# Performance work log

Hardware: AMD Instinct MI355X
Metric: run time of the kernel (lower is better)

## Reference

```python
import jax, jax.numpy as jnp
import numpy as np

N = 20000; E = 160000; C = 64; SH = 9; NB = 8
S_DIM = 16; MS_HID = 64; FC_HID = 64
RATE = 0.1; LAMBDA = 0.5; R_MAX = 5.0; EV_PER = 16
K = int(RATE * N)          # static master-node count (top-k selection)
E_V = EV_PER * K           # static virtual-edge budget


def _safe_len(vec):
    # smooth norm, safe under autodiff at zero-length edges (self loops)
    return jnp.sqrt(jnp.sum(vec * vec, axis=-1, keepdims=True) + 1e-12)


def _sh(vec):
    # real spherical harmonics lmax=2, 'component' normalization, on unit vectors
    n = vec / _safe_len(vec)
    x, y, z = n[:, 0], n[:, 1], n[:, 2]
    s3 = jnp.sqrt(3.0); s15 = jnp.sqrt(15.0); s5 = jnp.sqrt(5.0)
    return jnp.stack([
        jnp.ones_like(x),
        s3 * x, s3 * y, s3 * z,
        s15 * x * y, s15 * y * z, 0.5 * s5 * (3 * z * z - 1.0),
        s15 * x * z, 0.5 * s15 * (x * x - y * y),
    ], axis=-1)  # [E, 9]


def _bessel(r):
    # Bessel radial basis with p=6 polynomial cutoff envelope; r: [E,1]
    n = jnp.arange(1, NB + 1, dtype=r.dtype)
    b = jnp.sqrt(2.0 / R_MAX) * jnp.sin(n * jnp.pi * r / R_MAX) / jnp.clip(r, 1e-9)
    u = jnp.clip(r / R_MAX, 0.0, 1.0); p = 6.0
    env = 1.0 - (p + 1) * (p + 2) / 2 * u ** p + p * (p + 2) * u ** (p + 1) - p * (p + 1) / 2 * u ** (p + 2)
    return b * env  # [E, NB]


def _conv(h, src, dst, sh, ef, emask, n_nodes, fc_w1, fc_b1, fc_w2, fc_b2, lin_w):
    # TFN-style tensor-product conv: per-edge weights from radial MLP,
    # message = flatten(h[dst] outer sh) * w -> linear -> scatter-mean to src
    w = jax.nn.relu(ef @ fc_w1 + fc_b1) @ fc_w2 + fc_b2            # [E, C*SH]
    tp = (h[dst][:, :, None] * sh[:, None, :]).reshape(sh.shape[0], -1) * w
    msg = (tp @ lin_w) * emask[:, None]                            # [E, C]
    agg = jax.ops.segment_sum(msg, src, num_segments=n_nodes)
    deg = jax.ops.segment_sum(emask, src, num_segments=n_nodes)
    return agg / jnp.clip(deg, 1.0)[:, None]


def setup_inputs() -> dict:
    key = jax.random.key(0)
    ks = jax.random.split(key, 12)
    def lin(k, i, o):
        return (jax.random.normal(k, (i, o), jnp.float32) / np.sqrt(i)).astype(jnp.float32)
    return {
        "h": jax.random.normal(ks[0], (N, C), jnp.float32),
        "pos": jax.random.uniform(ks[1], (N, 3), jnp.float32) * 10.0,
        "edge_index": jax.random.randint(ks[2], (2, E), 0, N, dtype=jnp.int32),
        "fc_w1": lin(ks[3], NB, FC_HID), "fc_b1": jnp.zeros((FC_HID,), jnp.float32),
        "fc_w2": lin(ks[4], FC_HID, C * SH), "fc_b2": jnp.zeros((C * SH,), jnp.float32),
        "lin_w": lin(ks[5], C * SH, C),
        "ms_w1": lin(ks[6], S_DIM, MS_HID), "ms_b1": jnp.zeros((MS_HID,), jnp.float32),
        "ms_w2": lin(ks[7], MS_HID, 1), "ms_b2": jnp.zeros((1,), jnp.float32),
        "vg_wq": lin(ks[8], S_DIM, S_DIM), "vg_wk": lin(ks[9], S_DIM, S_DIM),
    }


def reference(h, pos, fc_w1, fc_b1, fc_w2, fc_b2, lin_w,
              ms_w1, ms_b1, ms_w2, ms_b2, vg_wq, vg_wk, edge_index):
    src, dst = edge_index[0], edge_index[1]
    vec = pos[src] - pos[dst]
    sh = _sh(vec)
    ef = _bessel(_safe_len(vec))
    ones_e = jnp.ones((E,), h.dtype)
    h_update = _conv(h, src, dst, sh, ef, ones_e, N, fc_w1, fc_b1, fc_w2, fc_b2, lin_w)
    h_local = h_update + h  # in_dim == out_dim -> pad is a no-op

    # --- master selection (top-k by learned score; static K) ---
    h_sc = h_local[:, :S_DIM]
    score = jax.nn.sigmoid(
        (jax.nn.relu(h_sc @ ms_w1 + ms_b1) @ ms_w2 + ms_b2).squeeze(-1))  # [N]
    _, top_idx = jax.lax.top_k(score, K)
    node_mask = jnp.zeros((N,), h.dtype).at[top_idx].set(1.0)
    m = score * node_mask
    master_idx = jnp.sort(top_idx)

    # relabel full-graph ids -> master-subgraph ids (masked subgraph extraction)
    node2m = jnp.full((N,), -1, jnp.int32).at[master_idx].set(jnp.arange(K, dtype=jnp.int32))
    src_m, dst_m = node2m[src], node2m[dst]
    e_mask = ((src_m >= 0) & (dst_m >= 0)).astype(h.dtype)
    src_mc = jnp.where(src_m >= 0, src_m, 0)
    dst_mc = jnp.where(dst_m >= 0, dst_m, 0)
    adj = jnp.zeros((K, K), h.dtype).at[src_mc, dst_mc].add(e_mask)

    h_master = h_local[master_idx]
    pos_master = pos[master_idx]
    h_ms = h_master[:, :S_DIM]

    # --- virtual edge generation (attention, thresholded by lambda) ---
    q = h_ms @ vg_wq; kk = h_ms @ vg_wk
    attn = jax.nn.sigmoid(q @ kk.T / np.sqrt(S_DIM))  # [K, K]
    exist = (adj > 0) | jnp.eye(K, dtype=bool)
    A_virtual = jnp.where((~exist) & (attn > LAMBDA), 1.0, 0.0).astype(h.dtype)
    vvals, vidx = jax.lax.top_k((attn * A_virtual).reshape(-1), E_V)
    v_src = (vidx // K).astype(jnp.int32); v_dst = (vidx % K).astype(jnp.int32)
    v_mask = (vvals > 0).astype(h.dtype)

    src_all = jnp.concatenate([src_mc, v_src])
    dst_all = jnp.concatenate([dst_mc, v_dst])
    mask_all = jnp.concatenate([e_mask, v_mask])
    vec_m = pos_master[src_all] - pos_master[dst_all]
    sh_m = _sh(vec_m)
    ef_m = _bessel(_safe_len(vec_m))
    h_m_update = _conv(h_master, src_all, dst_all, sh_m, ef_m, mask_all, K,
                       fc_w1, fc_b1, fc_w2, fc_b2, lin_w)
    h_hier = h_m_update + h_master

    h_hier_exp = jnp.zeros_like(h_local).at[master_idx].set(h_hier)
    m_e = m[:, None]
    h_final = (1.0 - m_e) * h_local + m_e * h_hier_exp
    return (h_final, pos, A_virtual, m)
```

## Files before the change

kernel.cpp:

```cpp
#include <hip/hip_runtime.h>
#include <stdint.h>

constexpr int N_   = 20000;
constexpr int E_   = 160000;
constexpr int C_   = 64;
constexpr int K_   = 2000;
constexpr int EV_  = 32000;
constexpr int EALL_ = E_ + EV_;
constexpr int CSH_ = 576;
constexpr int TB_  = 64;
constexpr int NFLAT_ = K_ * K_;

constexpr size_t OFF_AGG    = 0;
constexpr size_t OFF_DEG    = 5120000;
constexpr size_t OFF_AGGM   = 5200000;
constexpr size_t OFF_DEGM   = 5712000;
constexpr size_t OFF_RANK   = 5720000;
constexpr size_t OFF_MASKA  = 5800000;
constexpr size_t OFF_EXIST  = 6568000;
constexpr size_t OFF_HIST   = 10568000;
constexpr size_t OFF_STATE  = 10572096;
constexpr size_t OFF_HLOCAL = 10572352;
constexpr size_t OFF_KEY    = 15692352;
constexpr size_t OFF_SCORE  = 15852352;
constexpr size_t OFF_N2M    = 15932352;
constexpr size_t OFF_MIDX   = 16012352;
constexpr size_t OFF_HM     = 16020352;
constexpr size_t OFF_POSM   = 16532352;
constexpr size_t OFF_Q      = 16556352;
constexpr size_t OFF_KBUF   = 16684352;
constexpr size_t OFF_SRCA   = 16812352;
constexpr size_t OFF_DSTA   = 17580352;
constexpr size_t OFF_WMAX   = 18348352;
constexpr size_t OFF_CAND   = 18598400;

struct RState {
    unsigned long long prefix;
    int R;
    unsigned int cand_count;
    unsigned int sel_count;
    int bin_thresh;
    unsigned int total;
    unsigned int pad;
};

__global__ __launch_bounds__(256) void k_init(const float* __restrict__ fc_b1,
    const float* __restrict__ fc_w2, const float* __restrict__ fc_b2, char* __restrict__ ws)
{
    float4 zero4 = make_float4(0.f, 0.f, 0.f, 0.f);
    float4* z = (float4*)ws;
    int nz4 = (int)(OFF_STATE / 16);
    for (int i = blockIdx.x * 256 + threadIdx.x; i < nz4; i += gridDim.x * 256) z[i] = zero4;
    if (blockIdx.x == gridDim.x - 1) {
        __shared__ float hid0[64];
        __shared__ int nz;
        int t = threadIdx.x;
        float4* zs = (float4*)(ws + OFF_STATE);
        if (t < 16) zs[t] = zero4;
        if (t == 0) nz = 0;
        if (t < 64) hid0[t] = fmaxf(fc_b1[t], 0.0f);
        __syncthreads();
        for (int j = t; j < CSH_; j += 256) {
            float acc = fc_b2[j];
            for (int k = 0; k < 64; k++) acc += hid0[k] * fc_w2[k * CSH_ + j];
            if (acc != 0.0f) atomicOr(&nz, 1);
        }
        __syncthreads();
        if (t == 0) *(int*)(ws + OFF_STATE + 72) = nz;
    }
}

__global__ __launch_bounds__(256) void k_prep(
    int n_edges, const int* __restrict__ src, const int* __restrict__ dst,
    const float* __restrict__ mask, const float* __restrict__ posn,
    const int* __restrict__ w0nz, float* __restrict__ deg,
    float* __restrict__ edata, unsigned int* __restrict__ cnt)
{
    int e = blockIdx.x * 256 + threadIdx.x;
    bool valid = e < n_edges;
    int s_i = 0, d_i = 0; float msk = 0.0f;
    if (valid) {
        msk = mask ? mask[e] : 1.0f;
        if (msk != 0.0f) { s_i = src[e]; d_i = dst[e]; }
    }
    bool active = valid && (msk != 0.0f);

    float vx = 0.f, vy = 0.f, vz = 0.f;
    if (active) {
        vx = posn[s_i*3+0] - posn[d_i*3+0];
        vy = posn[s_i*3+1] - posn[d_i*3+1];
        vz = posn[s_i*3+2] - posn[d_i*3+2];
    }
    float r = sqrtf(vx*vx + vy*vy + vz*vz + 1e-12f);
    float invr = 1.0f / r;
    float x = vx*invr, y = vy*invr, z = vz*invr;
    const float s3 = 1.7320508075688772f, s15 = 3.872983346207417f, s5 = 2.23606797749979f;
    float sh[9];
    sh[0] = 1.0f; sh[1] = s3*x; sh[2] = s3*y; sh[3] = s3*z;
    sh[4] = s15*x*y; sh[5] = s15*y*z; sh[6] = 0.5f*s5*(3.0f*z*z - 1.0f);
    sh[7] = s15*x*z; sh[8] = 0.5f*s15*(x*x - y*y);

    float u = r * 0.2f; u = u > 1.0f ? 1.0f : u;
    float u2 = u*u, u6 = u2*u2*u2, u7 = u6*u, u8 = u7*u;
    float env = 1.0f - 28.0f*u6 + 48.0f*u7 - 21.0f*u8;
    float rc = r > 1e-9f ? r : 1e-9f;
    const float bpref = 0.6324555320336759f;
    const float PIov5 = 0.6283185307179586f;
    float ef[8];
    #pragma unroll
    for (int n = 0; n < 8; n++)
        ef[n] = bpref * sinf(PIov5 * r * (float)(n + 1)) / rc * env;

    if (active) atomicAdd(&deg[s_i], msk);

    bool contrib = active && !((env == 0.0f) && (*w0nz == 0));
    int lane = threadIdx.x & 63;
    unsigned long long b = __ballot(contrib);
    int wc = __popcll(b);
    int base = 0;
    if (lane == 0 && wc) base = (int)atomicAdd(cnt, (unsigned)wc);
    base = __shfl(base, 0);
    if (contrib) {
        int slot = base + __popcll(b & ((1ull << lane) - 1ull));
        float* p = edata + (size_t)slot * 20;
        #pragma unroll
        for (int n = 0; n < 8; n++) p[n] = ef[n];
        #pragma unroll
        for (int t = 0; t < 9; t++) p[8+t] = sh[t];
        p[17] = __int_as_float(s_i);
        p[18] = __int_as_float(d_i);
        p[19] = msk;
    }
}

__global__ __launch_bounds__(256, 3) void k_convg(
    const unsigned int* __restrict__ cnt, const float* __restrict__ edata,
    const float* __restrict__ hn,
    const float* __restrict__ fc_w1, const float* __restrict__ fc_b1,
    const float* __restrict__ fc_w2, const float* __restrict__ fc_b2,
    const float* __restrict__ lin_w, float* __restrict__ agg)
{
    __shared__ float s_misc[TB_ * 12];
    __shared__ __align__(16) float s_hid[64 * 64];
    __shared__ __align__(16) float s_tp[64 * 68];
    __shared__ __align__(16) float s_w[4096];

    const int tid = threadIdx.x;
    const int oq = (tid & 15) * 4;
    const int e0 = (tid >> 4) * 4;

    const int nheavy = (int)*cnt;
    const int nblk = (nheavy + TB_ - 1) / TB_;

    for (int blk = blockIdx.x; blk < nblk; blk += gridDim.x) {
        const int ebase = blk * TB_;
        int nE = nheavy - ebase; if (nE > TB_) nE = TB_;

        __syncthreads();
        for (int idx = tid; idx < TB_ * 12; idx += 256) {
            int e = idx / 12, f = idx - 12 * e;
            float v = 0.0f;
            if (e < nE) {
                const float* p = edata + (size_t)(ebase + e) * 20;
                v = (f < 9) ? p[8 + f] : (f == 9) ? p[17] : (f == 10) ? p[19] : p[18];
            }
            s_misc[idx] = v;
        }
        for (int idx = tid; idx < TB_ * 64; idx += 256) {
            int k = idx >> 6, e = idx & 63;
            float hv = 0.0f;
            if (e < nE) {
                const float* p = edata + (size_t)(ebase + e) * 20;
                float acc = fc_b1[k];
                #pragma unroll
                for (int n = 0; n < 8; n++) acc += p[n] * fc_w1[n * 64 + k];
                hv = fmaxf(acc, 0.0f);
            }
            s_hid[k * 64 + e] = hv;
        }
        float acc[4][4] = {{0,0,0,0},{0,0,0,0},{0,0,0,0},{0,0,0,0}};
        __syncthreads();

        const int d0 = __float_as_int(s_misc[(e0+0) * 12 + 11]);
        const int d1 = __float_as_int(s_misc[(e0+1) * 12 + 11]);
        const int d2 = __float_as_int(s_misc[(e0+2) * 12 + 11]);
        const int d3 = __float_as_int(s_misc[(e0+3) * 12 + 11]);

        for (int cj = 0; cj < 9; cj++) {
            const int j0 = cj * 64;
            if (cj) __syncthreads();
            for (int i4 = tid; i4 < 1024; i4 += 256) {
                int k = i4 >> 4, q4 = (i4 & 15) * 4;
                *reinterpret_cast<float4*>(&s_w[k * 64 + q4]) =
                    *reinterpret_cast<const float4*>(&fc_w2[k * CSH_ + j0 + q4]);
            }
            __syncthreads();

            const int jb = j0 + oq;
            const int c0 = jb / 9, c1 = (jb + 3) / 9;
            float hA0 = hn[d0 * 64 + c0], hB0 = hn[d0 * 64 + c1];
            float hA1 = hn[d1 * 64 + c0], hB1 = hn[d1 * 64 + c1];
            float hA2 = hn[d2 * 64 + c0], hB2 = hn[d2 * 64 + c1];
            float hA3 = hn[d3 * 64 + c0], hB3 = hn[d3 * 64 + c1];

            float a[4][4];
            #pragma unroll
            for (int q = 0; q < 4; q++) {
                float b = fc_b2[jb + q];
                a[0][q]=b; a[1][q]=b; a[2][q]=b; a[3][q]=b;
            }
            #pragma unroll 4
            for (int k = 0; k < 64; k++) {
                float4 w4 = *reinterpret_cast<const float4*>(&s_w[k * 64 + oq]);
                float4 h4 = *reinterpret_cast<const float4*>(&s_hid[k * 64 + e0]);
                a[0][0]+=h4.x*w4.x; a[0][1]+=h4.x*w4.y; a[0][2]+=h4.x*w4.z; a[0][3]+=h4.x*w4.w;
                a[1][0]+=h4.y*w4.x; a[1][1]+=h4.y*w4.y; a[1][2]+=h4.y*w4.z; a[1][3]+=h4.y*w4.w;
                a[2][0]+=h4.z*w4.x; a[2][1]+=h4.z*w4.y; a[2][2]+=h4.z*w4.z; a[2][3]+=h4.z*w4.w;
                a[3][0]+=h4.w*w4.x; a[3][1]+=h4.w*w4.y; a[3][2]+=h4.w*w4.z; a[3][3]+=h4.w*w4.w;
            }
            #pragma unroll
            for (int q = 0; q < 4; q++) {
                int j = jb + q; int cc = j / 9; int si = j - 9 * cc;
                float4 tpv;
                tpv.x = (cc == c0 ? hA0 : hB0) * s_misc[(e0+0) * 12 + si] * a[0][q];
                tpv.y = (cc == c0 ? hA1 : hB1) * s_misc[(e0+1) * 12 + si] * a[1][q];
                tpv.z = (cc == c0 ? hA2 : hB2) * s_misc[(e0+2) * 12 + si] * a[2][q];
                tpv.w = (cc == c0 ? hA3 : hB3) * s_misc[(e0+3) * 12 + si] * a[3][q];
                *reinterpret_cast<float4*>(&s_tp[(oq + q) * 68 + e0]) = tpv;
            }
            __syncthreads();

            for (int i4 = tid; i4 < 1024; i4 += 256) {
                *reinterpret_cast<float4*>(&s_w[i4 * 4]) =
                    *reinterpret_cast<const float4*>(&lin_w[j0 * 64 + i4 * 4]);
            }
            __syncthreads();

            #pragma unroll 4
            for (int jj = 0; jj < 64; jj++) {
                float4 l4 = *reinterpret_cast<const float4*>(&s_w[jj * 64 + oq]);
                float4 t4 = *reinterpret_cast<const float4*>(&s_tp[jj * 68 + e0]);
                acc[0][0]+=t4.x*l4.x; acc[0][1]+=t4.x*l4.y; acc[0][2]+=t4.x*l4.z; acc[0][3]+=t4.x*l4.w;
                acc[1][0]+=t4.y*l4.x; acc[1][1]+=t4.y*l4.y; acc[1][2]+=t4.y*l4.z; acc[1][3]+=t4.y*l4.w;
                acc[2][0]+=t4.z*l4.x; acc[2][1]+=t4.z*l4.y; acc[2][2]+=t4.z*l4.z; acc[2][3]+=t4.z*l4.w;
                acc[3][0]+=t4.w*l4.x; acc[3][1]+=t4.w*l4.y; acc[3][2]+=t4.w*l4.z; acc[3][3]+=t4.w*l4.w;
            }
        }

        #pragma unroll
        for (int t = 0; t < 4; t++) {
            float mk = s_misc[(e0+t) * 12 + 10];
            if (mk != 0.0f) {
                int s = __float_as_int(s_misc[(e0+t) * 12 + 9]);
                #pragma unroll
                for (int q = 0; q < 4; q++) atomicAdd(&agg[s * 64 + oq + q], acc[t][q] * mk);
            }
        }
    }
}

__global__ __launch_bounds__(256) void k_hlscore(const float* __restrict__ h,
    const float* __restrict__ agg, const float* __restrict__ deg,
    const float* __restrict__ ms_w1, const float* __restrict__ ms_b1,
    const float* __restrict__ ms_w2, const float* __restrict__ ms_b2,
    float* __restrict__ h_local, float* __restrict__ score, unsigned long long* __restrict__ key)
{
    int wid = threadIdx.x >> 6, lane = threadIdx.x & 63;
    int n = blockIdx.x * 4 + wid;
    if (n >= N_) return;
    float d = fmaxf(deg[n], 1.0f);
    float hl = h[n*64 + lane] + agg[n*64 + lane] / d;
    h_local[n*64 + lane] = hl;
    float acc = ms_b1[lane];
    #pragma unroll
    for (int i = 0; i < 16; i++) acc += __shfl(hl, i) * ms_w1[i*64 + lane];
    acc = fmaxf(acc, 0.0f);
    float part = acc * ms_w2[lane];
    #pragma unroll
    for (int off = 32; off > 0; off >>= 1) part += __shfl_xor(part, off);
    if (lane == 0) {
        float s = part + ms_b2[0];
        float sc = 1.0f / (1.0f + expf(-s));
        score[n] = sc;
        key[n] = ((unsigned long long)__float_as_uint(sc) << 32)
               | (unsigned long long)(0xFFFFFFFFu - (unsigned)n);
    }
}

__global__ __launch_bounds__(256) void k_rank(const unsigned long long* __restrict__ key,
                                              int* __restrict__ rankcnt)
{
    int i = blockIdx.x * 256 + threadIdx.x;
    int seg = blockIdx.y;
    int lo = seg * 1250, hi = lo + 1250;
    unsigned long long my = (i < N_) ? key[i] : ~0ull;
    int cnt = 0;
    #pragma unroll 8
    for (int j = lo; j < hi; j++) cnt += (key[j] > my) ? 1 : 0;
    if (i < N_ && cnt) atomicAdd(&rankcnt[i], cnt);
}

__global__ __launch_bounds__(1024) void k_scanfin(const int* __restrict__ rankcnt,
    const float* __restrict__ score, int* __restrict__ node2m, int* __restrict__ midx,
    float* __restrict__ m_out)
{
    __shared__ int wsum[16];
    __shared__ int wbase[16];
    __shared__ int s_base;
    int tid = threadIdx.x, lane = tid & 63, wv = tid >> 6;
    if (tid == 0) s_base = 0;
    __syncthreads();
    for (int c = 0; c < 20; c++) {
        int idx = c * 1024 + tid;
        int sel = 0;
        if (idx < N_) {
            sel = (rankcnt[idx] < K_) ? 1 : 0;
            m_out[idx] = sel ? score[idx] : 0.0f;
        }
        int v = sel;
        #pragma unroll
        for (int off = 1; off < 64; off <<= 1) {
            int u = __shfl_up(v, off);
            if (lane >= off) v += u;
        }
        if (lane == 63) wsum[wv] = v;
        __syncthreads();
        if (tid == 0) {
            int runb = s_base;
            for (int w = 0; w < 16; w++) { wbase[w] = runb; runb += wsum[w]; }
            s_base = runb;
        }
        __syncthreads();
        if (idx < N_) {
            if (sel) { int rk = wbase[wv] + v - 1; node2m[idx] = rk; midx[rk] = idx; }
            else node2m[idx] = -1;
        }
    }
}

__global__ __launch_bounds__(256) void k_mastex(const int* __restrict__ midx,
    const float* __restrict__ h_local, const float* __restrict__ pos,
    const float* __restrict__ vg_wq, const float* __restrict__ vg_wk,
    const int* __restrict__ src, const int* __restrict__ dst, const int* __restrict__ node2m,
    float* __restrict__ h_m, float* __restrict__ pos_m,
    float* __restrict__ qbuf, float* __restrict__ kbuf,
    int* __restrict__ src_all, int* __restrict__ dst_all,
    float* __restrict__ mask_all, unsigned char* __restrict__ exist)
{
    int b = blockIdx.x;
    if (b < 500) {
        int mi = b * 4 + (threadIdx.x >> 6);
        int lane = threadIdx.x & 63;
        int node = midx[mi];
        h_m[mi*64 + lane] = h_local[node*64 + lane];
        if (lane < 3) pos_m[mi*3 + lane] = pos[node*3 + lane];
        if (lane < 32) {
            int j = lane & 15;
            const float* wm = (lane < 16) ? vg_wq : vg_wk;
            float acc = 0.0f;
            #pragma unroll
            for (int i = 0; i < 16; i++) acc += h_local[node*64 + i] * wm[i*16 + j];
            if (lane < 16) qbuf[mi*16 + j] = acc; else kbuf[mi*16 + j] = acc;
        }
    } else {
        int e = (b - 500) * 256 + threadIdx.x;
        int sm = node2m[src[e]], dm = node2m[dst[e]];
        bool em = (sm >= 0) && (dm >= 0);
        int smc = sm >= 0 ? sm : 0;
        int dmc = dm >= 0 ? dm : 0;
        src_all[e] = smc; dst_all[e] = dmc; mask_all[e] = em ? 1.0f : 0.0f;
        if (em) exist[smc * K_ + dmc] = 1;
    }
}

__global__ __launch_bounds__(256) void k_attn1(const float* __restrict__ qbuf,
    const float* __restrict__ kbuf, const unsigned char* __restrict__ exist,
    float* __restrict__ Av, float* __restrict__ wmax, unsigned int* __restrict__ hist,
    RState* st, unsigned int* __restrict__ done_ctr)
{
    __shared__ unsigned int lh[1024];
    __shared__ unsigned int ha[1024], hb[1024];
    __shared__ unsigned int s_last;
    int tid = threadIdx.x, lane = tid & 63;
    for (int b = tid; b < 1024; b += 256) lh[b] = 0;
    __syncthreads();

    const int stride = gridDim.x * 256;
    for (int flat = blockIdx.x * 256 + tid; flat < NFLAT_; flat += stride) {
        int gi = flat / K_;
        int gj = flat - gi * K_;
        const float4* qp = reinterpret_cast<const float4*>(qbuf + gi * 16);
        const float4* kp = reinterpret_cast<const float4*>(kbuf + gj * 16);
        float dot = 0.0f;
        #pragma unroll
        for (int c4 = 0; c4 < 4; c4++) {
            float4 q4 = qp[c4], k4 = kp[c4];
            dot += q4.x*k4.x + q4.y*k4.y + q4.z*k4.z + q4.w*k4.w;
        }
        float attn = 1.0f / (1.0f + expf(-dot * 0.25f));
        bool ex = (exist[flat] != 0) || (gi == gj);
        bool av = (!ex) && (attn > 0.5f);
        Av[flat] = av ? 1.0f : 0.0f;
        float cv = av ? attn : 0.0f;
        if (av) {
            unsigned bin = (__float_as_uint(attn) - 0x3F000000u) >> 13;
            if (bin > 1023u) bin = 1023u;
            atomicAdd(&lh[bin], 1u);
        }
        float wm = cv;
        #pragma unroll
        for (int off = 32; off > 0; off >>= 1) wm = fmaxf(wm, __shfl_xor(wm, off));
        if (lane == 0) wmax[flat >> 6] = wm;
    }
    __syncthreads();
    for (int b = tid; b < 1024; b += 256) {
        unsigned v = lh[b];
        if (v) atomicAdd(&hist[b], v);
    }
    __syncthreads();
    __threadfence();
    if (tid == 0) s_last = (atomicAdd(done_ctr, 1u) == (unsigned)gridDim.x - 1u) ? 1u : 0u;
    __syncthreads();
    if (!s_last) return;
    __threadfence();
    for (int b = tid; b < 1024; b += 256) ha[b] = atomicAdd(&hist[b], 0u);
    __syncthreads();
    unsigned* srcp = ha; unsigned* dstp = hb;
    for (int off = 1; off < 1024; off <<= 1) {
        for (int b = tid; b < 1024; b += 256)
            dstp[b] = srcp[b] + ((b + off < 1024) ? srcp[b + off] : 0u);
        __syncthreads();
        unsigned* tmp = srcp; srcp = dstp; dstp = tmp;
    }
    unsigned total = srcp[0];
    int R = (total < (unsigned)EV_) ? (int)total : EV_;
    if (tid == 0) {
        st->R = R; st->total = total; st->cand_count = 0; st->sel_count = 0;
        if (R == 0) st->bin_thresh = 1024;
    }
    __syncthreads();
    if (R > 0) {
        for (int b = tid; b < 1024; b += 256) {
            unsigned hi2 = (b == 1023) ? 0u : srcp[b + 1];
            if ((int)srcp[b] >= R && (int)hi2 < R) st->bin_thresh = b;
        }
    }
}

__global__ __launch_bounds__(256) void k_attn2(const float* __restrict__ qbuf,
    const float* __restrict__ kbuf, const unsigned char* __restrict__ exist,
    const float* __restrict__ wmax, RState* st, unsigned long long* __restrict__ cand)
{
    __shared__ int wb[4];
    __shared__ int bb;
    int tid = threadIdx.x, lane = tid & 63, wv = tid >> 6;
    unsigned tbits = 0x3F000000u + ((unsigned)st->bin_thresh << 13);
    const int stride = gridDim.x * 256;

    for (int base = blockIdx.x * 256; base < NFLAT_; base += stride) {
        int flat = base + tid;
        bool wactive = __float_as_uint(wmax[(base + wv * 64) >> 6]) >= tbits;
        bool store = false;
        unsigned long long keyv = 0ull;
        if (wactive) {
            int gi = flat / K_;
            int gj = flat - gi * K_;
            const float4* qp = reinterpret_cast<const float4*>(qbuf + gi * 16);
            const float4* kp = reinterpret_cast<const float4*>(kbuf + gj * 16);
            float dot = 0.0f;
            #pragma unroll
            for (int c4 = 0; c4 < 4; c4++) {
                float4 q4 = qp[c4], k4 = kp[c4];
                dot += q4.x*k4.x + q4.y*k4.y + q4.z*k4.z + q4.w*k4.w;
            }
            float attn = 1.0f / (1.0f + expf(-dot * 0.25f));
            bool ex = (exist[flat] != 0) || (gi == gj);
            store = (!ex) && (attn > 0.5f) && (__float_as_uint(attn) >= tbits);
            keyv = ((unsigned long long)__float_as_uint(attn) << 32)
                 | (unsigned long long)(0xFFFFFFFFu - (unsigned)flat);
        }
        unsigned long long b = __ballot(store);
        int wc = __popcll(b);
        if (lane == 0) wb[wv] = wc;
        __syncthreads();
        if (tid == 0) {
            int s = 0;
            for (int w = 0; w < 4; w++) { int cc2 = wb[w]; wb[w] = s; s += cc2; }
            bb = s ? (int)atomicAdd(&st->cand_count, (unsigned)s) : 0;
        }
        __syncthreads();
        if (store) {
            int slot = bb + wb[wv] + __popcll(b & ((1ull << lane) - 1ull));
            cand[slot] = keyv;
        }
        __syncthreads();
    }
}

__global__ __launch_bounds__(1024) void k_radixsel(RState* st,
    const unsigned long long* __restrict__ cand,
    int* __restrict__ src_all, int* __restrict__ dst_all, float* __restrict__ mask_all)
{
    __shared__ unsigned int lh[256];
    __shared__ unsigned int suf[256];
    __shared__ unsigned int s_tie[8192];
    __shared__ unsigned int s_pref, s_R, s_tiecnt, s_cfth;
    int tid = threadIdx.x;
    int n = (int)st->cand_count;
    int R = st->R;
    if (tid == 0) { s_pref = 0x3F000000u; s_R = (unsigned)R; s_tiecnt = 0; s_cfth = 0; }
    __syncthreads();

    unsigned long long T;
    if (R > 0) {
        for (int p = 0; p < 3; p++) {
            if (tid < 256) lh[tid] = 0;
            __syncthreads();
            unsigned pref = s_pref;
            int sh_d = 16 - 8 * p;
            unsigned pm = 0xFFFFFFFFu << (sh_d + 8);
            for (int i = tid; i < n; i += 1024) {
                unsigned a = (unsigned)(cand[i] >> 32);
                if ((a & pm) == (pref & pm))
                    atomicAdd(&lh[(a >> sh_d) & 255u], 1u);
            }
            __syncthreads();
            if (tid < 256) suf[tid] = lh[tid];
            __syncthreads();
            for (int off = 1; off < 256; off <<= 1) {
                unsigned v = 0;
                if (tid < 256 && tid + off < 256) v = suf[tid + off];
                __syncthreads();
                if (tid < 256) suf[tid] += v;
                __syncthreads();
            }
            if (tid < 256) {
                unsigned Rc = s_R;
                unsigned hi2 = (tid == 255) ? 0u : suf[tid + 1];
                if (suf[tid] >= Rc && hi2 < Rc) {
                    s_pref = pref | ((unsigned)tid << sh_d);
                    s_R = Rc - hi2;
                }
            }
            __syncthreads();
        }
        unsigned Ta = s_pref;
        unsigned Rrem = s_R;
        for (int i = tid; i < n; i += 1024) {
            unsigned long long kv = cand[i];
            if ((unsigned)(kv >> 32) == Ta) {
                unsigned pos = atomicAdd(&s_tiecnt, 1u);
                if (pos < 8192u) s_tie[pos] = (unsigned)(kv & 0xFFFFFFFFull);
            }
        }
        __syncthreads();
        unsigned Cq = s_tiecnt; if (Cq > 8192u) Cq = 8192u;
        if (Rrem >= 1u && Rrem < Cq) {
            for (int i = tid; i < (int)Cq; i += 1024) {
                unsigned me = s_tie[i];
                unsigned r = 0;
                for (int j = 0; j < (int)Cq; j++) r += (s_tie[j] > me) ? 1u : 0u;
                if (r == Rrem - 1u) s_cfth = me;
            }
        }
        __syncthreads();
        T = ((unsigned long long)Ta << 32) | (unsigned long long)s_cfth;
    } else {
        T = ~0ull;
    }

    int lane = tid & 63;
    for (int i0 = 0; i0 < n; i0 += 1024) {
        int i = i0 + tid;
        bool sel = (i < n) && (cand[i] >= T);
        unsigned long long b = __ballot(sel);
        int wc = __popcll(b);
        int basep = 0;
        if (lane == 0 && wc) basep = (int)atomicAdd(&st->sel_count, (unsigned)wc);
        basep = __shfl(basep, 0);
        if (sel) {
            int slot = basep + __popcll(b & ((1ull << lane) - 1ull));
            if (slot < EV_) {
                unsigned flat = 0xFFFFFFFFu - (unsigned)(cand[i] & 0xFFFFFFFFull);
                src_all[E_ + slot] = (int)(flat / (unsigned)K_);
                dst_all[E_ + slot] = (int)(flat % (unsigned)K_);
                mask_all[E_ + slot] = 1.0f;
            }
        }
    }
}

__global__ void k_finalpos(const float* __restrict__ h_local, const int* __restrict__ node2m,
    const float* __restrict__ aggm, const float* __restrict__ degm, const float* __restrict__ h_m,
    const float* __restrict__ m_out, const float* __restrict__ pos,
    float* __restrict__ out_h, float* __restrict__ out_pos)
{
    int idx = blockIdx.x * 256 + threadIdx.x;
    if (idx < N_ * 3) out_pos[idx] = pos[idx];
    if (idx >= N_ * C_) return;
    int i = idx >> 6, c = idx & 63;
    float mval = m_out[i];
    int mi = node2m[i];
    float hh = 0.0f;
    if (mi >= 0) hh = aggm[mi*64 + c] / fmaxf(degm[mi], 1.0f) + h_m[mi*64 + c];
    out_h[idx] = (1.0f - mval) * h_local[idx] + mval * hh;
}

extern "C" void kernel_launch(void* const* d_in, const int* in_sizes, int n_in,
                              void* d_out, int out_size, void* d_ws, size_t ws_size,
                              hipStream_t stream)
{
    (void)in_sizes; (void)n_in; (void)out_size; (void)ws_size;
    const float* h     = (const float*)d_in[0];
    const float* pos   = (const float*)d_in[1];
    const int*   eidx  = (const int*)d_in[2];
    const float* fc_w1 = (const float*)d_in[3];
    const float* fc_b1 = (const float*)d_in[4];
    const float* fc_w2 = (const float*)d_in[5];
    const float* fc_b2 = (const float*)d_in[6];
    const float* lin_w = (const float*)d_in[7];
    const float* ms_w1 = (const float*)d_in[8];
    const float* ms_b1 = (const float*)d_in[9];
    const float* ms_w2 = (const float*)d_in[10];
    const float* ms_b2 = (const float*)d_in[11];
    const float* vg_wq = (const float*)d_in[12];
    const float* vg_wk = (const float*)d_in[13];

    char* ws = (char*)d_ws;
    float* agg     = (float*)(ws + OFF_AGG);
    float* deg     = (float*)(ws + OFF_DEG);
    float* aggm    = (float*)(ws + OFF_AGGM);
    float* degm    = (float*)(ws + OFF_DEGM);
    int*   rankcnt = (int*)(ws + OFF_RANK);
    float* mask_all = (float*)(ws + OFF_MASKA);
    unsigned char* exist = (unsigned char*)(ws + OFF_EXIST);
    unsigned int* hist = (unsigned int*)(ws + OFF_HIST);
    RState* st     = (RState*)(ws + OFF_STATE);
    unsigned int* cnt0 = (unsigned int*)(ws + OFF_STATE + 64);
    unsigned int* cnt1 = (unsigned int*)(ws + OFF_STATE + 68);
    int*   w0nz    = (int*)(ws + OFF_STATE + 72);
    unsigned int* done_a1 = (unsigned int*)(ws + OFF_STATE + 76);
    float* h_local = (float*)(ws + OFF_HLOCAL);
    unsigned long long* key = (unsigned long long*)(ws + OFF_KEY);
    float* score   = (float*)(ws + OFF_SCORE);
    int*   node2m  = (int*)(ws + OFF_N2M);
    int*   midx    = (int*)(ws + OFF_MIDX);
    float* h_m     = (float*)(ws + OFF_HM);
    float* pos_m   = (float*)(ws + OFF_POSM);
    float* qbuf    = (float*)(ws + OFF_Q);
    float* kbuf    = (float*)(ws + OFF_KBUF);
    int*   src_all = (int*)(ws + OFF_SRCA);
    int*   dst_all = (int*)(ws + OFF_DSTA);
    float* wmax    = (float*)(ws + OFF_WMAX);
    unsigned long long* cand = (unsigned long long*)(ws + OFF_CAND);
    float* edata   = (float*)(ws + OFF_CAND);

    float* out_h   = (float*)d_out;
    float* out_pos = out_h + (size_t)N_ * C_;
    float* out_av  = out_pos + (size_t)N_ * 3;
    float* out_m   = out_av + (size_t)K_ * K_;

    k_init<<<768, 256, 0, stream>>>(fc_b1, fc_w2, fc_b2, ws);

    k_prep<<<E_ / 256, 256, 0, stream>>>(E_, eidx, eidx + E_, nullptr, pos, w0nz, deg, edata, cnt0);
    k_convg<<<768, 256, 0, stream>>>(cnt0, edata, h, fc_w1, fc_b1, fc_w2, fc_b2, lin_w, agg);

    k_hlscore<<<(N_ + 3) / 4, 256, 0, stream>>>(h, agg, deg, ms_w1, ms_b1, ms_w2, ms_b2,
                                                h_local, score, key);

    k_rank<<<dim3((N_ + 255) / 256, 16), 256, 0, stream>>>(key, rankcnt);
    k_scanfin<<<1, 1024, 0, stream>>>(rankcnt, score, node2m, midx, out_m);

    k_mastex<<<500 + E_ / 256, 256, 0, stream>>>(midx, h_local, pos, vg_wq, vg_wk,
        eidx, eidx + E_, node2m, h_m, pos_m, qbuf, kbuf, src_all, dst_all, mask_all, exist);

    k_attn1<<<1024, 256, 0, stream>>>(qbuf, kbuf, exist, out_av, wmax, hist, st, done_a1);
    k_attn2<<<1024, 256, 0, stream>>>(qbuf, kbuf, exist, wmax, st, cand);
    k_radixsel<<<1, 1024, 0, stream>>>(st, cand, src_all, dst_all, mask_all);

    k_prep<<<EALL_ / 256, 256, 0, stream>>>(EALL_, src_all, dst_all, mask_all, pos_m, w0nz,
                                            degm, edata, cnt1);
    k_convg<<<768, 256, 0, stream>>>(cnt1, edata, h_m, fc_w1, fc_b1, fc_w2, fc_b2, lin_w, aggm);

    k_finalpos<<<(N_ * C_ + 255) / 256, 256, 0, stream>>>(h_local, node2m, aggm, degm, h_m,
                                                          out_m, pos, out_h, out_pos);
}
```

Before: 714.8 us.

## Fuse rank+scan and attn2+radix-select via last-block-done pattern

Merges the rank-count kernel with the single-block prefix-scan, and the candidate-collection kernel with the single-block radix select. In each pair the last block to finish, detected with a global atomic counter, runs the serial tail. This removes two kernel launches and their inter-kernel gaps, and the rank scan now has each thread process 79 contiguous nodes. In exchange, the tail runs with only 256 threads instead of 1024 and uses atomic reads for coherence, which may slow the serial phase. It also depends on the done counters being reset in the workspace init.

```diff
diff --git a/kernel.cpp b/kernel.cpp
--- a/kernel.cpp
+++ b/kernel.cpp
@@ -287,52 +287,63 @@
     }
 }
 
-__global__ __launch_bounds__(256) void k_rank(const unsigned long long* __restrict__ key,
-                                              int* __restrict__ rankcnt)
-{
-    int i = blockIdx.x * 256 + threadIdx.x;
-    int seg = blockIdx.y;
-    int lo = seg * 1250, hi = lo + 1250;
-    unsigned long long my = (i < N_) ? key[i] : ~0ull;
-    int cnt = 0;
-    #pragma unroll 8
-    for (int j = lo; j < hi; j++) cnt += (key[j] > my) ? 1 : 0;
-    if (i < N_ && cnt) atomicAdd(&rankcnt[i], cnt);
-}
-
-__global__ __launch_bounds__(1024) void k_scanfin(const int* __restrict__ rankcnt,
-    const float* __restrict__ score, int* __restrict__ node2m, int* __restrict__ midx,
-    float* __restrict__ m_out)
-{
-    __shared__ int wsum[16];
-    __shared__ int wbase[16];
-    __shared__ int s_base;
+__global__ __launch_bounds__(256) void k_rankscan(const unsigned long long* __restrict__ key,
+    int* __restrict__ rankcnt, const float* __restrict__ score,
+    int* __restrict__ node2m, int* __restrict__ midx, float* __restrict__ m_out,
+    unsigned int* __restrict__ done)
+{
     int tid = threadIdx.x, lane = tid & 63, wv = tid >> 6;
-    if (tid == 0) s_base = 0;
-    __syncthreads();
-    for (int c = 0; c < 20; c++) {
-        int idx = c * 1024 + tid;
-        int sel = 0;
+    {
+        int ib = blockIdx.x % 79;
+        int seg = blockIdx.x / 79;
+        int i = ib * 256 + tid;
+        int lo = seg * 1250, hi = lo + 1250;
+        unsigned long long my = (i < N_) ? key[i] : ~0ull;
+        int cnt = 0;
+        #pragma unroll 8
+        for (int j = lo; j < hi; j++) cnt += (key[j] > my) ? 1 : 0;
+        if (i < N_ && cnt) atomicAdd(&rankcnt[i], cnt);
+    }
+    __threadfence();
+    __syncthreads();
+    __shared__ unsigned int s_last;
+    if (tid == 0) s_last = (atomicAdd(done, 1u) == (unsigned)gridDim.x - 1u) ? 1u : 0u;
+    __syncthreads();
+    if (!s_last) return;
+    __threadfence();
+
+    const int base = tid * 79;
+    unsigned long long m0 = 0ull; unsigned m1 = 0u;
+    int csel = 0;
+    for (int k = 0; k < 79; k++) {
+        int idx = base + k;
         if (idx < N_) {
-            sel = (rankcnt[idx] < K_) ? 1 : 0;
+            int r = atomicAdd(&rankcnt[idx], 0);
+            int sel = (r < K_) ? 1 : 0;
             m_out[idx] = sel ? score[idx] : 0.0f;
-        }
-        int v = sel;
-        #pragma unroll
-        for (int off = 1; off < 64; off <<= 1) {
-            int u = __shfl_up(v, off);
-            if (lane >= off) v += u;
-        }
-        if (lane == 63) wsum[wv] = v;
-        __syncthreads();
-        if (tid == 0) {
-            int runb = s_base;
-            for (int w = 0; w < 16; w++) { wbase[w] = runb; runb += wsum[w]; }
-            s_base = runb;
-        }
-        __syncthreads();
+            if (sel) {
+                if (k < 64) m0 |= (1ull << k); else m1 |= (1u << (k - 64));
+                csel++;
+            }
+        }
+    }
+    __shared__ int wsum[4], wbase[4];
+    int v = csel;
+    #pragma unroll
+    for (int off = 1; off < 64; off <<= 1) {
+        int u = __shfl_up(v, off);
+        if (lane >= off) v += u;
+    }
+    if (lane == 63) wsum[wv] = v;
+    __syncthreads();
+    if (tid == 0) { int run = 0; for (int w = 0; w < 4; w++) { int c = wsum[w]; wbase[w] = run; run += c; } }
+    __syncthreads();
+    int run = wbase[wv] + v - csel;
+    for (int k = 0; k < 79; k++) {
+        int idx = base + k;
         if (idx < N_) {
-            if (sel) { int rk = wbase[wv] + v - 1; node2m[idx] = rk; midx[rk] = idx; }
+            bool sel = (k < 64) ? ((m0 >> k) & 1ull) : ((m1 >> (k - 64)) & 1u);
+            if (sel) { node2m[idx] = run; midx[run] = idx; run++; }
             else node2m[idx] = -1;
         }
     }
@@ -447,12 +458,15 @@
     }
 }
 
-__global__ __launch_bounds__(256) void k_attn2(const float* __restrict__ qbuf,
+__global__ __launch_bounds__(256) void k_attn2rs(const float* __restrict__ qbuf,
     const float* __restrict__ kbuf, const unsigned char* __restrict__ exist,
-    const float* __restrict__ wmax, RState* st, unsigned long long* __restrict__ cand)
+    const float* __restrict__ wmax, RState* st, unsigned long long* __restrict__ cand,
+    int* __restrict__ src_all, int* __restrict__ dst_all, float* __restrict__ mask_all,
+    unsigned int* __restrict__ done)
 {
     __shared__ int wb[4];
     __shared__ int bb;
+    __shared__ unsigned int s_last;
     int tid = threadIdx.x, lane = tid & 63, wv = tid >> 6;
     unsigned tbits = 0x3F000000u + ((unsigned)st->bin_thresh << 13);
     const int stride = gridDim.x * 256;
@@ -491,88 +505,89 @@
         __syncthreads();
         if (store) {
             int slot = bb + wb[wv] + __popcll(b & ((1ull << lane) - 1ull));
-            cand[slot] = keyv;
-        }
-        __syncthreads();
-    }
-}
-
-__global__ __launch_bounds__(1024) void k_radixsel(RState* st,
-    const unsigned long long* __restrict__ cand,
-    int* __restrict__ src_all, int* __restrict__ dst_all, float* __restrict__ mask_all)
-{
-    __shared__ unsigned int lh[256];
+            atomicExch(&cand[slot], keyv);
+        }
+        __syncthreads();
+    }
+
+    __threadfence();
+    __syncthreads();
+    if (tid == 0) s_last = (atomicAdd(done, 1u) == (unsigned)gridDim.x - 1u) ? 1u : 0u;
+    __syncthreads();
+    if (!s_last) return;
+    __threadfence();
+
+    __shared__ unsigned int lh2[256];
     __shared__ unsigned int suf[256];
     __shared__ unsigned int s_tie[8192];
-    __shared__ unsigned int s_pref, s_R, s_tiecnt, s_cfth;
-    int tid = threadIdx.x;
-    int n = (int)st->cand_count;
+    __shared__ unsigned int scal[4];
+    int n = (int)atomicAdd(&st->cand_count, 0u);
     int R = st->R;
-    if (tid == 0) { s_pref = 0x3F000000u; s_R = (unsigned)R; s_tiecnt = 0; s_cfth = 0; }
+    if (tid == 0) { scal[0] = 0x3F000000u; scal[1] = (unsigned)R; scal[2] = 0; scal[3] = 0; }
     __syncthreads();
 
     unsigned long long T;
     if (R > 0) {
-        for (int p = 0; p < 3; p++) {
-            if (tid < 256) lh[tid] = 0;
+        for (int pss = 0; pss < 3; pss++) {
+            lh2[tid] = 0;
             __syncthreads();
-            unsigned pref = s_pref;
-            int sh_d = 16 - 8 * p;
+            unsigned pref = scal[0];
+            int sh_d = 16 - 8 * pss;
             unsigned pm = 0xFFFFFFFFu << (sh_d + 8);
-            for (int i = tid; i < n; i += 1024) {
-                unsigned a = (unsigned)(cand[i] >> 32);
+            for (int i = tid; i < n; i += 256) {
+                unsigned long long kv = atomicAdd(&cand[i], 0ull);
+                unsigned a = (unsigned)(kv >> 32);
                 if ((a & pm) == (pref & pm))
-                    atomicAdd(&lh[(a >> sh_d) & 255u], 1u);
+                    atomicAdd(&lh2[(a >> sh_d) & 255u], 1u);
             }
             __syncthreads();
-            if (tid < 256) suf[tid] = lh[tid];
+            suf[tid] = lh2[tid];
             __syncthreads();
             for (int off = 1; off < 256; off <<= 1) {
-                unsigned v = 0;
-                if (tid < 256 && tid + off < 256) v = suf[tid + off];
+                unsigned v = (tid + off < 256) ? suf[tid + off] : 0u;
                 __syncthreads();
-                if (tid < 256) suf[tid] += v;
+                suf[tid] += v;
                 __syncthreads();
             }
-            if (tid < 256) {
-                unsigned Rc = s_R;
+            {
+                unsigned Rc = scal[1];
                 unsigned hi2 = (tid == 255) ? 0u : suf[tid + 1];
                 if (suf[tid] >= Rc && hi2 < Rc) {
-                    s_pref = pref | ((unsigned)tid << sh_d);
-                    s_R = Rc - hi2;
+                    scal[0] = pref | ((unsigned)tid << sh_d);
+                    scal[1] = Rc - hi2;
                 }
             }
             __syncthreads();
         }
-        unsigned Ta = s_pref;
-        unsigned Rrem = s_R;
-        for (int i = tid; i < n; i += 1024) {
-            unsigned long long kv = cand[i];
+        unsigned Ta = scal[0];
+        unsigned Rrem = scal[1];
+        for (int i = tid; i < n; i += 256) {
+            unsigned long long kv = atomicAdd(&cand[i], 0ull);
             if ((unsigned)(kv >> 32) == Ta) {
-                unsigned pos = atomicAdd(&s_tiecnt, 1u);
+                unsigned pos = atomicAdd(&scal[2], 1u);
                 if (pos < 8192u) s_tie[pos] = (unsigned)(kv & 0xFFFFFFFFull);
             }
         }
         __syncthreads();
-        unsigned Cq = s_tiecnt; if (Cq > 8192u) Cq = 8192u;
+        unsigned Cq = scal[2]; if (Cq > 8192u) Cq = 8192u;
         if (Rrem >= 1u && Rrem < Cq) {
-            for (int i = tid; i < (int)Cq; i += 1024) {
+            for (int i = tid; i < (int)Cq; i += 256) {
                 unsigned me = s_tie[i];
                 unsigned r = 0;
                 for (int j = 0; j < (int)Cq; j++) r += (s_tie[j] > me) ? 1u : 0u;
-                if (r == Rrem - 1u) s_cfth = me;
-            }
-        }
-        __syncthreads();
-        T = ((unsigned long long)Ta << 32) | (unsigned long long)s_cfth;
+                if (r == Rrem - 1u) scal[3] = me;
+            }
+        }
+        __syncthreads();
+        T = ((unsigned long long)Ta << 32) | (unsigned long long)scal[3];
     } else {
         T = ~0ull;
     }
 
-    int lane = tid & 63;
-    for (int i0 = 0; i0 < n; i0 += 1024) {
+    for (int i0 = 0; i0 < n; i0 += 256) {
         int i = i0 + tid;
-        bool sel = (i < n) && (cand[i] >= T);
+        unsigned long long kv = (i < n) ? atomicAdd(&cand[i], 0ull) : 0ull;
+        bool sel = (i < n) && (kv >= T);
         unsigned long long b = __ballot(sel);
         int wc = __popcll(b);
         int basep = 0;
@@ -581,7 +596,7 @@
         if (sel) {
             int slot = basep + __popcll(b & ((1ull << lane) - 1ull));
             if (slot < EV_) {
-                unsigned flat = 0xFFFFFFFFu - (unsigned)(cand[i] & 0xFFFFFFFFull);
+                unsigned flat = 0xFFFFFFFFu - (unsigned)(kv & 0xFFFFFFFFull);
                 src_all[E_ + slot] = (int)(flat / (unsigned)K_);
                 dst_all[E_ + slot] = (int)(flat % (unsigned)K_);
                 mask_all[E_ + slot] = 1.0f;
@@ -640,6 +655,8 @@
     unsigned int* cnt1 = (unsigned int*)(ws + OFF_STATE + 68);
     int*   w0nz    = (int*)(ws + OFF_STATE + 72);
     unsigned int* done_a1 = (unsigned int*)(ws + OFF_STATE + 76);
+    unsigned int* done_rk = (unsigned int*)(ws + OFF_STATE + 80);
+    unsigned int* done_a2 = (unsigned int*)(ws + OFF_STATE + 84);
     float* h_local = (float*)(ws + OFF_HLOCAL);
     unsigned long long* key = (unsigned long long*)(ws + OFF_KEY);
     float* score   = (float*)(ws + OFF_SCORE);
@@ -668,15 +685,14 @@
     k_hlscore<<<(N_ + 3) / 4, 256, 0, stream>>>(h, agg, deg, ms_w1, ms_b1, ms_w2, ms_b2,
                                                 h_local, score, key);
 
-    k_rank<<<dim3((N_ + 255) / 256, 16), 256, 0, stream>>>(key, rankcnt);
-    k_scanfin<<<1, 1024, 0, stream>>>(rankcnt, score, node2m, midx, out_m);
+    k_rankscan<<<79 * 16, 256, 0, stream>>>(key, rankcnt, score, node2m, midx, out_m, done_rk);
 
     k_mastex<<<500 + E_ / 256, 256, 0, stream>>>(midx, h_local, pos, vg_wq, vg_wk,
         eidx, eidx + E_, node2m, h_m, pos_m, qbuf, kbuf, src_all, dst_all, mask_all, exist);
 
     k_attn1<<<1024, 256, 0, stream>>>(qbuf, kbuf, exist, out_av, wmax, hist, st, done_a1);
-    k_attn2<<<1024, 256, 0, stream>>>(qbuf, kbuf, exist, wmax, st, cand);
-    k_radixsel<<<1, 1024, 0, stream>>>(st, cand, src_all, dst_all, mask_all);
+    k_attn2rs<<<1024, 256, 0, stream>>>(qbuf, kbuf, exist, wmax, st, cand,
+                                        src_all, dst_all, mask_all, done_a2);
 
     k_prep<<<EALL_ / 256, 256, 0, stream>>>(EALL_, src_all, dst_all, mask_all, pos_m, w0nz,
                                             degm, edata, cnt1);
```

Result: slower. 980.0 us (+37.1%).
